# Performance work log

Measured on AMD Instinct MI355X. Metric: run time of the kernel, lower is better.

The kernel has to match this reference:

```python
import jax, jax.numpy as jnp
import numpy as np

NEG = -jnp.inf


def _pipeline(logits, presence_penalties, frequency_penalties, repetition_penalties,
              temperatures, top_p, min_p, top_a, tfs, typical_p,
              epsilon_cutoff, eta_cutoff, smoothing_factor, smoothing_curve,
              prompt_tokens, output_tokens, top_k):
    N, V = logits.shape
    rows = jnp.arange(N)[:, None]
    cols = jnp.arange(V)[None, :]

    # ---- presence / frequency / repetition penalties (bincount via scatter-add) ----
    pbin = jnp.zeros((N, V + 1), jnp.int32).at[rows, prompt_tokens].add(1)[:, :V]
    obin = jnp.zeros((N, V + 1), jnp.int32).at[rows, output_tokens].add(1)[:, :V]
    seen = (pbin > 0) | (obin > 0)
    rp = jnp.where(seen, repetition_penalties[:, None], 1.0)
    logits = jnp.where(logits > 0, logits / rp, logits * rp)
    logits = logits - frequency_penalties[:, None] * obin.astype(logits.dtype)
    logits = logits - presence_penalties[:, None] * (obin > 0).astype(logits.dtype)

    # ---- temperature ----
    logits = logits / temperatures[:, None]

    # ---- top-k + top-p (sort ascending, mask, unsort) ----
    order = jnp.argsort(logits, axis=-1)               # ascending
    ls = jnp.take_along_axis(logits, order, axis=-1)
    kth_pos = (V - jnp.clip(top_k.astype(jnp.int32), 1, V))[:, None]
    kth_val = jnp.take_along_axis(ls, kth_pos, axis=1)
    ls = jnp.where(ls < kth_val, NEG, ls)
    cs = jnp.cumsum(jax.nn.softmax(ls, axis=-1), axis=-1)
    pmask = (cs <= (1.0 - top_p)[:, None]).at[:, -1].set(False)
    ls = jnp.where(pmask, NEG, ls)
    logits = jnp.take_along_axis(ls, jnp.argsort(order, axis=-1), axis=-1)

    # ---- tail-free sampling (sort descending, 2nd-derivative CDF cutoff) ----
    order_d = jnp.argsort(-logits, axis=-1)            # descending order of logits
    ls = jnp.take_along_axis(logits, order_d, axis=-1)
    probs = jax.nn.softmax(ls, axis=-1)
    d2 = jnp.abs(jnp.diff(jnp.diff(probs, axis=-1), axis=-1))   # (N, V-2)
    cdf = jnp.cumsum(d2 / jnp.sum(d2, axis=-1, keepdims=True), axis=-1)
    m = cdf > tfs[:, None]
    m = jnp.concatenate([jnp.zeros((N, 1), bool), m, jnp.ones((N, 1), bool)], axis=-1)
    ls = jnp.where(m, NEG, ls)
    logits = jnp.take_along_axis(ls, jnp.argsort(order_d, axis=-1), axis=-1)

    # ---- eta cutoff (entropy-adaptive threshold, always keep argmax) ----
    sl = jax.nn.log_softmax(logits, axis=-1)
    probs = jnp.exp(sl)
    sl_safe = jnp.where(probs > 0, sl, 0.0)            # nansum equivalent
    neg_ent = jnp.sum(probs * sl_safe, axis=-1)
    eps = jnp.minimum(eta_cutoff, jnp.sqrt(eta_cutoff) * jnp.exp(neg_ent))[:, None]
    top_idx = jnp.argmax(probs, axis=-1)[:, None]
    logits = jnp.where((probs < eps) & (cols != top_idx), NEG, logits)

    # ---- epsilon cutoff (absolute prob threshold, always keep argmax) ----
    probs = jax.nn.softmax(logits, axis=-1)
    top_idx = jnp.argmax(probs, axis=-1)[:, None]
    logits = jnp.where((probs < epsilon_cutoff[:, None]) & (cols != top_idx), NEG, logits)

    # ---- locally typical sampling ----
    sl = jax.nn.log_softmax(logits, axis=-1)
    probs = jnp.exp(sl)
    sl_safe = jnp.where(probs > 0, sl, 0.0)
    neg_ent = jnp.sum(probs * sl_safe, axis=-1, keepdims=True)
    dev = jnp.abs(neg_ent - sl)                        # surprisal deviation
    order_t = jnp.argsort(dev, axis=-1)
    rp2 = jnp.take_along_axis(probs, order_t, axis=-1)
    msort = (jnp.cumsum(rp2, axis=-1) >= typical_p[:, None]).at[:, 0].set(False)
    mask = jnp.zeros((N, V), bool).at[rows, order_t].set(msort)
    logits = jnp.where(mask, NEG, logits)

    # ---- quadratic (smoothing) sampling ----
    mx = jnp.max(logits, axis=-1, keepdims=True)
    finite = logits != NEG
    diff = jnp.where(finite, logits, mx) - mx          # finite everywhere
    kq = (3.0 - smoothing_curve[:, None]) / 2.0
    sq = (smoothing_curve[:, None] - 1.0) / 2.0
    sfc = smoothing_factor[:, None]
    trans = -(kq * sfc * diff ** 2) + sq * sfc * diff ** 3 + mx
    trans = jnp.where(finite, trans, logits)
    logits = jnp.where(sfc > 0, trans, logits)

    # ---- min-p ----
    probs = jax.nn.softmax(logits, axis=-1)
    top_prob = jnp.max(probs, axis=-1, keepdims=True)
    logits = jnp.where(probs < min_p[:, None] * top_prob, NEG, logits)

    # ---- top-a ----
    probs = jax.nn.softmax(logits, axis=-1)
    top_prob = jnp.max(probs, axis=-1, keepdims=True)
    logits = jnp.where(probs < top_a[:, None] * top_prob ** 2, NEG, logits)

    return logits


def setup_inputs() -> dict:
    N, V, PL, OL = 256, 50257, 512, 128
    ks = jax.random.split(jax.random.key(0), 17)
    u = lambda k, lo, hi: lo + (hi - lo) * jax.random.uniform(k, (N,), jnp.float32)
    return {
        "logits": 3.0 * jax.random.normal(ks[0], (N, V), jnp.float32),
        "prompt_tokens": jax.random.randint(ks[1], (N, PL), 0, V),
        "output_tokens": jax.random.randint(ks[2], (N, OL), 0, V),
        "presence_penalties": u(ks[3], 0.0, 0.5),
        "frequency_penalties": u(ks[4], 0.0, 0.5),
        "repetition_penalties": u(ks[5], 1.0, 1.3),
        "temperatures": u(ks[6], 0.5, 1.5),
        "top_p": u(ks[7], 0.85, 0.99),
        "top_k": jax.random.randint(ks[8], (N,), 1, 2048, dtype=jnp.int32),
        "min_p": u(ks[9], 0.0, 0.05),
        "top_a": u(ks[10], 0.0, 0.1),
        "tfs": u(ks[11], 0.95, 0.999),
        "typical_p": u(ks[12], 0.9, 0.999),
        "epsilon_cutoff": u(ks[13], 1e-5, 1e-4),
        "eta_cutoff": u(ks[14], 1e-5, 1e-4),
        "smoothing_factor": u(ks[15], 0.05, 0.25),
        "smoothing_curve": u(ks[16], 1.0, 2.0),
    }


def reference(logits, prompt_tokens, output_tokens, presence_penalties,
              frequency_penalties, repetition_penalties, temperatures, top_p,
              top_k, min_p, top_a, tfs, typical_p, epsilon_cutoff, eta_cutoff,
              smoothing_factor, smoothing_curve):
    return _pipeline(logits, presence_penalties, frequency_penalties,
                     repetition_penalties, temperatures, top_p, min_p, top_a,
                     tfs, typical_p, epsilon_cutoff, eta_cutoff,
                     smoothing_factor, smoothing_curve,
                     prompt_tokens, output_tokens, top_k)
```

## Files before the change

### kernel.cpp

```cpp
#include <hip/hip_runtime.h>
#include <stdint.h>

#define TPB 1024
#define NWAVE 16
#define MAXK 2304
#define NV4 13
#define BIG_NEG (-1.0e30f)

__device__ __forceinline__ uint32_t fkey(float x) {
  uint32_t s = __float_as_uint(x);
  return (s & 0x80000000u) ? ~s : (s | 0x80000000u);
}
__device__ __forceinline__ float fkey_inv(uint32_t u) {
  uint32_t s = (u & 0x80000000u) ? (u & 0x7fffffffu) : ~u;
  return __uint_as_float(s);
}
__device__ __forceinline__ unsigned long long shfl_xor_u64(unsigned long long v, int m) {
  uint32_t lo = (uint32_t)v, hi = (uint32_t)(v >> 32);
  lo = (uint32_t)__shfl_xor((int)lo, m, 64);
  hi = (uint32_t)__shfl_xor((int)hi, m, 64);
  return (((unsigned long long)hi) << 32) | lo;
}

struct TokMem { uint32_t obin[12568]; uint32_t seen[1600]; };
struct SortMem { unsigned long long kp[4096]; };
union __align__(16) U1 { TokMem tok; SortMem srt; };

__device__ __forceinline__ float block_sum1(float v, float* buf) {
  int lane = threadIdx.x & 63, wd = threadIdx.x >> 6;
#pragma unroll
  for (int off = 32; off > 0; off >>= 1) v += __shfl_down(v, off, 64);
  if (lane == 0) buf[wd] = v;
  __syncthreads();
  const float4* b4 = (const float4*)buf;
  float4 A = b4[0], B = b4[1], C = b4[2], D = b4[3];
  float r = A.x; r += A.y; r += A.z; r += A.w;
  r += B.x; r += B.y; r += B.z; r += B.w;
  r += C.x; r += C.y; r += C.z; r += C.w;
  r += D.x; r += D.y; r += D.z; r += D.w;
  return r;
}

__device__ __forceinline__ float wbuf_prefix(const float* wbuf, int wd) {
  const float4* w4 = (const float4*)wbuf;
  float4 a = w4[0], b = w4[1], c = w4[2], d = w4[3];
  float t[16] = {a.x, a.y, a.z, a.w, b.x, b.y, b.z, b.w,
                 c.x, c.y, c.z, c.w, d.x, d.y, d.z, d.w};
  float base = 0.f;
#pragma unroll
  for (int i = 0; i < 16; ++i) base += (i < wd) ? t[i] : 0.f;
  return base;
}

__device__ __forceinline__ int wave_reduce_int(int v) {
#pragma unroll
  for (int off = 32; off > 0; off >>= 1) v += __shfl_down(v, off, 64);
  return __shfl(v, 0, 64);
}

template <class Pred>
__device__ __forceinline__ int wave_psearch(int lo, int hi, Pred pred) {
  const int lane = (int)threadIdx.x & 63;
  while (lo <= hi) {
    int range = hi - lo + 1;
    int stride = (range + 63) >> 6;
    long long p = (long long)lo + (long long)stride * lane;
    bool q = (p <= hi) ? pred((int)p) : false;
    unsigned long long bm = __ballot(q);
    int h = bm ? (63 - (int)__clzll(bm)) : -1;
    int nlo = (h >= 0) ? (int)((long long)lo + (long long)stride * h + 1) : lo;
    long long pf = (long long)lo + (long long)stride * (h + 1);
    int nhi = (pf <= (long long)hi) ? (int)pf - 1 : hi;
    if (nlo > nhi) return nlo;
    lo = nlo; hi = nhi;
  }
  return lo;
}

__device__ void block_scan3x3(const float* __restrict__ se, float* __restrict__ sp,
                              float* __restrict__ sq, float* __restrict__ sr, int m,
                              float* wA, float* wB, float* wC) {
  int tid = (int)threadIdx.x, lane = tid & 63, wd = tid >> 6;
  int b = tid * 3;
  __syncthreads();
  float e0 = (b     < m) ? se[b]     : 0.f;
  float e1 = (b + 1 < m) ? se[b + 1] : 0.f;
  float e2 = (b + 2 < m) ? se[b + 2] : 0.f;
  float e3 = (b + 3 < m) ? se[b + 3] : 0.f;
  float e4 = (b + 4 < m) ? se[b + 4] : 0.f;
  float q0 = (b     < m) ? sq[b]     : 0.f;
  float q1 = (b + 1 < m) ? sq[b + 1] : 0.f;
  float q2 = (b + 2 < m) ? sq[b + 2] : 0.f;
  float z0 = fabsf((e2 - e1) - (e1 - e0));
  float z1 = fabsf((e3 - e2) - (e2 - e1));
  float z2 = fabsf((e4 - e3) - (e3 - e2));
  float ae1 = e0 + e1, ae2 = ae1 + e2;
  float aq1 = q0 + q1, aq2 = aq1 + q2;
  float az1 = z0 + z1, az2 = az1 + z2;
  float tE = ae2, wE = ae2, tQ = aq2, wQ = aq2, tZ = az2, wZ = az2;
#pragma unroll
  for (int off = 1; off < 64; off <<= 1) {
    float sE = __shfl_up(wE, off, 64);
    float sQ = __shfl_up(wQ, off, 64);
    float sZ = __shfl_up(wZ, off, 64);
    if (lane >= off) { wE += sE; wQ += sQ; wZ += sZ; }
  }
  if (lane == 63) { wA[wd] = wE; wB[wd] = wQ; wC[wd] = wZ; }
  __syncthreads();
  float bE = wbuf_prefix(wA, wd), bQ = wbuf_prefix(wB, wd), bZ = wbuf_prefix(wC, wd);
  float xE = bE + (wE - tE), xQ = bQ + (wQ - tQ), xZ = bZ + (wZ - tZ);
  if (b < m)     { sp[b]     = e0 + xE;  sq[b]     = q0 + xQ;  sr[b]     = z0 + xZ; }
  if (b + 1 < m) { sp[b + 1] = ae1 + xE; sq[b + 1] = aq1 + xQ; sr[b + 1] = az1 + xZ; }
  if (b + 2 < m) { sp[b + 2] = ae2 + xE; sq[b + 2] = aq2 + xQ; sr[b + 2] = az2 + xZ; }
  __syncthreads();
}

__device__ uint32_t wave_select_digit2k(const uint32_t* __restrict__ h, uint32_t* w_io) {
  int lane = threadIdx.x & 63;
  uint32_t w = *w_io;
  const int base = lane << 5;
  uint32_t lsum = 0;
#pragma unroll
  for (int t = 0; t < 8; ++t) {
    const int tt = (t + lane) & 7;
    const uint4 v = *(const uint4*)(h + base + tt * 4);
    lsum += v.x + v.y + v.z + v.w;
  }
  uint32_t W = lsum;
#pragma unroll
  for (int off = 1; off < 64; off <<= 1) {
    uint32_t x = (uint32_t)__shfl_down((int)W, off, 64);
    if (lane + off < 64) W += x;
  }
  uint32_t Wn = (uint32_t)__shfl_down((int)W, 1, 64);
  if (lane == 63) Wn = 0;
  const bool isb = (W >= w) && (Wn < w);
  int dloc = -1; uint32_t wloc = 0;
  if (isb) {
    uint32_t sfx = Wn;
#pragma unroll
    for (int t = 31; t >= 0; --t) {
      uint32_t c = h[base + t];
      uint32_t si = sfx + c;
      if (si >= w && sfx < w) { dloc = base + t; wloc = w - sfx; }
      sfx = si;
    }
  }
  unsigned long long bm = __ballot(dloc >= 0);
  int src = (int)__popcll(bm - 1ull);
  uint32_t d = (uint32_t)__shfl(dloc, src, 64);
  *w_io = (uint32_t)__shfl((int)wloc, src, 64);
  return d;
}

__device__ uint32_t wave_select_digit256(const uint32_t* __restrict__ h, uint32_t* w_io) {
  int lane = threadIdx.x & 63;
  uint32_t w = *w_io;
  const uint4 v = ((const uint4*)h)[lane];
  uint32_t c0 = v.x, c1 = v.y, c2 = v.z, c3 = v.w;
  uint32_t t0 = c0 + c1 + c2 + c3;
  uint32_t W = t0;
#pragma unroll
  for (int off = 1; off < 64; off <<= 1) {
    uint32_t x = (uint32_t)__shfl_down((int)W, off, 64);
    if (lane + off < 64) W += x;
  }
  uint32_t Wn = (uint32_t)__shfl_down((int)W, 1, 64);
  if (lane == 63) Wn = 0;
  uint32_t S0 = W, S1 = W - c0, S2 = S1 - c1, S3 = S2 - c2, S4 = Wn;
  int dloc = -1; uint32_t wloc = 0;
  if (S0 >= w && S1 < w) { dloc = 4 * lane + 0; wloc = w - S1; }
  if (S1 >= w && S2 < w) { dloc = 4 * lane + 1; wloc = w - S2; }
  if (S2 >= w && S3 < w) { dloc = 4 * lane + 2; wloc = w - S3; }
  if (S3 >= w && S4 < w) { dloc = 4 * lane + 3; wloc = w - S4; }
  unsigned long long bm = __ballot(dloc >= 0);
  int src = (int)__popcll(bm - 1ull);
  uint32_t d = (uint32_t)__shfl(dloc, src, 64);
  *w_io = (uint32_t)__shfl((int)wloc, src, 64);
  return d;
}

template <int NE, bool PING>
__device__ void hybrid_sort(unsigned long long* kp, unsigned long long* kb1, int n) {
  const int tid = (int)threadIdx.x;
  unsigned long long k[NE];
#pragma unroll
  for (int e = 0; e < NE; ++e) {
    int i = e * TPB + tid;
    k[e] = (i < n) ? kp[i] : ~0ull;
  }
  int pb = 0;
  for (int kk = 2; kk <= n; kk <<= 1) {
    for (int j = kk >> 1; j > 0; j >>= 1) {
      if (j >= TPB) {
        const int em = j / TPB;
#pragma unroll
        for (int e = 0; e < NE; ++e) {
          if ((e & em) == 0 && (e + em) < NE) {
            int e2 = e + em;
            int i = e * TPB + tid;
            bool up = ((i & kk) == 0);
            if ((k[e] > k[e2]) == up) {
              unsigned long long tk = k[e]; k[e] = k[e2]; k[e2] = tk;
            }
          }
        }
      } else if (j >= 64) {
        unsigned long long* kb = (PING && pb) ? kb1 : kp;
#pragma unroll
        for (int e = 0; e < NE; ++e) {
          int i = e * TPB + tid;
          if (i < n) kb[i] = k[e];
        }
        __syncthreads();
#pragma unroll
        for (int e = 0; e < NE; ++e) {
          int i = e * TPB + tid;
          if (i < n) {
            unsigned long long o = kb[i ^ j];
            bool up = ((i & kk) == 0);
            bool lower = ((i & j) == 0);
            bool takeMin = (lower == up);
            bool takeOther = takeMin ? (o < k[e]) : (o > k[e]);
            if (takeOther) k[e] = o;
          }
        }
        if (PING) pb ^= 1;
        else __syncthreads();
      } else {
#pragma unroll
        for (int e = 0; e < NE; ++e) {
          int i = e * TPB + tid;
          unsigned long long o = shfl_xor_u64(k[e], j);
          bool up = ((i & kk) == 0);
          bool lower = ((i & j) == 0);
          bool takeMin = (lower == up);
          bool takeOther = takeMin ? (o < k[e]) : (o > k[e]);
          if (takeOther) k[e] = o;
        }
      }
    }
  }
  __syncthreads();
#pragma unroll
  for (int e = 0; e < NE; ++e) {
    int i = e * TPB + tid;
    if (i < n) kp[i] = k[e];
  }
  __syncthreads();
}

__device__ __forceinline__ uint32_t penal_val(float l, int j, bool sn,
    const uint32_t* __restrict__ obin,
    float f_rep, float inv_rep, float f_freq, float f_pres, float inv_temp) {
  int ob = 0;
  if (sn) ob = (int)((obin[j >> 2] >> (8 * (j & 3))) & 255u);
  l = (l > 0.0f) ? (l * (sn ? inv_rep : 1.0f)) : (l * (sn ? f_rep : 1.0f));
  l = l - f_freq * (float)ob;
  l = l - ((ob > 0) ? f_pres : 0.0f);
  l = l * inv_temp;
  return fkey(l);
}
__device__ __forceinline__ uint32_t penal_key(float l, int j,
    const uint32_t* __restrict__ seen, const uint32_t* __restrict__ obin,
    float f_rep, float inv_rep, float f_freq, float f_pres, float inv_temp) {
  bool sn = (seen[j >> 5] >> (j & 31)) & 1u;
  return penal_val(l, j, sn, obin, f_rep, inv_rep, f_freq, f_pres, inv_temp);
}

#define FOR_ELEMS(...) do {                                                   \
    if (tid < head) { int j = tid; uint32_t u = uh; (void)j; (void)u; __VA_ARGS__; } \
    _Pragma("unroll")                                                         \
    for (int s4_ = 0; s4_ < NV4; ++s4_) {                                     \
      int iv_ = s4_ * TPB + tid;                                              \
      if (iv_ < nvec) {                                                       \
        int jb_ = head + 4 * iv_;                                             \
        { int j = jb_ + 0; uint32_t u = uk[s4_ * 4 + 0]; (void)j; (void)u; __VA_ARGS__; } \
        { int j = jb_ + 1; uint32_t u = uk[s4_ * 4 + 1]; (void)j; (void)u; __VA_ARGS__; } \
        { int j = jb_ + 2; uint32_t u = uk[s4_ * 4 + 2]; (void)j; (void)u; __VA_ARGS__; } \
        { int j = jb_ + 3; uint32_t u = uk[s4_ * 4 + 3]; (void)j; (void)u; __VA_ARGS__; } \
      }                                                                       \
    }                                                                         \
    if (tid < ntail) { int j = head + 4 * nvec + tid; uint32_t u = ut; (void)j; (void)u; __VA_ARGS__; } \
  } while (0)

#define COLLECT_ELEM do {                                                     \
    bool pk_ = (u >= kth_u);                                                  \
    unsigned long long bm_ = __ballot(pk_);                                   \
    if (bm_) {                                                                \
      uint32_t base_ = 0;                                                     \
      if (lane == 0) base_ = atomicAdd(&s_cnt, (uint32_t)__popcll(bm_));      \
      base_ = (uint32_t)__shfl((int)base_, 0, 64);                            \
      if (pk_) {                                                              \
        uint32_t pos_ = base_ + (uint32_t)__popcll(bm_ & ((1ull << (unsigned)lane) - 1ull)); \
        if (pos_ < MAXK)                                                      \
          kp[pos_] = (((unsigned long long)(~u)) << 16) | (unsigned long long)(uint32_t)j; \
      }                                                                       \
    }                                                                         \
  } while (0)

__global__ __launch_bounds__(TPB, 4)
void sampler_kernel(const float* __restrict__ logits,
                    const int* __restrict__ ptoks, const int* __restrict__ otoks,
                    const float* __restrict__ pres, const float* __restrict__ freq,
                    const float* __restrict__ rep, const float* __restrict__ temp,
                    const float* __restrict__ topp, const int* __restrict__ topk,
                    const float* __restrict__ minp, const float* __restrict__ topa,
                    const float* __restrict__ tfsv, const float* __restrict__ typp,
                    const float* __restrict__ epsc, const float* __restrict__ etac,
                    const float* __restrict__ smf, const float* __restrict__ smc,
                    float* __restrict__ out, int N, int V, int PL, int OL) {
  __shared__ U1 u1;
  __shared__ __align__(16) uint32_t s_hist2k[2048];
  __shared__ __align__(16) uint32_t s_h256[256];
  __shared__ __align__(16) uint32_t s_h256b[256];
  __shared__ float s_e[MAXK];
  __shared__ float s_p[MAXK];
  __shared__ float s_q[MAXK];
  __shared__ float s_r[MAXK];
  __shared__ unsigned long long kb1[2048];
  __shared__ __align__(16) float s_site[12][NWAVE];
  __shared__ uint32_t s_cnt;
  __shared__ int s_K, s_ilo, s_ihi;

  const int tid = (int)threadIdx.x;
  const int r = (int)blockIdx.x;
  const int wd = tid >> 6;
  const int lane = tid & 63;

  const float* lrow = logits + (size_t)r * V;
  float* orow = out + (size_t)r * V;

  {
    const uint4 z4 = make_uint4(0u, 0u, 0u, 0u);
    uint4* ob4 = (uint4*)u1.tok.obin;
    for (int i = tid; i < 3142; i += TPB) ob4[i] = z4;
    uint4* se4 = (uint4*)u1.tok.seen;
    for (int i = tid; i < 400; i += TPB) se4[i] = z4;
    uint4* h4 = (uint4*)s_hist2k;
    for (int i = tid; i < 512; i += TPB) h4[i] = z4;
    if (tid < 64) ((uint4*)s_h256)[tid] = z4;
    else if (tid >= 64 && tid < 128) ((uint4*)s_h256b)[tid - 64] = z4;
  }
  if (tid == 0) s_cnt = 0;
  __syncthreads();
  for (int i = tid; i < PL; i += TPB) {
    int t = ptoks[(size_t)r * PL + i];
    if ((unsigned)t < (unsigned)V) atomicOr(&u1.tok.seen[t >> 5], 1u << (t & 31));
  }
  for (int i = tid; i < OL; i += TPB) {
    int t = otoks[(size_t)r * OL + i];
    if ((unsigned)t < (unsigned)V) {
      atomicOr(&u1.tok.seen[t >> 5], 1u << (t & 31));
      atomicAdd(&u1.tok.obin[t >> 2], 1u << (8 * (t & 3)));
    }
  }
  __syncthreads();

  const float f_pres = pres[r], f_freq = freq[r], f_rep = rep[r], f_temp = temp[r];
  const float f_topp = topp[r], f_minp = minp[r], f_topa = topa[r], f_tfs = tfsv[r];
  const float f_typp = typp[r], f_epsc = epsc[r], f_etac = etac[r];
  const float f_smf = smf[r], f_smc = smc[r];
  const float inv_rep = 1.0f / f_rep, inv_temp = 1.0f / f_temp;
  int k_topk = topk[r];
  if (k_topk < 1) k_topk = 1;
  if (k_topk > V) k_topk = V;

  const uint32_t* seenp = u1.tok.seen;
  const uint32_t* obinp = u1.tok.obin;

  uintptr_t ra = (uintptr_t)lrow;
  int head = (int)(((16u - (uint32_t)(ra & 15u)) & 15u) >> 2);
  if (head > V) head = V;
  const int nvec = (V - head) >> 2;
  const int ntail = V - head - (nvec << 2);

  uint32_t uk[NV4 * 4];
  uint32_t uh = 0, ut = 0;
#pragma unroll
  for (int s4 = 0; s4 < NV4; ++s4) {
    int iv = s4 * TPB + tid;
    uint32_t u0 = 0, u1k = 0, u2k = 0, u3 = 0;
    if (iv < nvec) {
      const float4 lv = *(const float4*)(lrow + head + 4 * iv);
      int jb = head + 4 * iv;
      uint32_t w0 = seenp[jb >> 5];
      uint32_t w1 = seenp[(jb >> 5) + 1];
      uint32_t sb = (uint32_t)(((((uint64_t)w1) << 32) | (uint64_t)w0) >> (jb & 31));
      u0 = penal_val(lv.x, jb + 0, (sb >> 0) & 1u, obinp, f_rep, inv_rep, f_freq, f_pres, inv_temp);
      u1k = penal_val(lv.y, jb + 1, (sb >> 1) & 1u, obinp, f_rep, inv_rep, f_freq, f_pres, inv_temp);
      u2k = penal_val(lv.z, jb + 2, (sb >> 2) & 1u, obinp, f_rep, inv_rep, f_freq, f_pres, inv_temp);
      u3 = penal_val(lv.w, jb + 3, (sb >> 3) & 1u, obinp, f_rep, inv_rep, f_freq, f_pres, inv_temp);
      atomicAdd(&s_hist2k[u0 >> 21], 1u);
      atomicAdd(&s_hist2k[u1k >> 21], 1u);
      atomicAdd(&s_hist2k[u2k >> 21], 1u);
      atomicAdd(&s_hist2k[u3 >> 21], 1u);
    }
    uk[s4 * 4 + 0] = u0; uk[s4 * 4 + 1] = u1k; uk[s4 * 4 + 2] = u2k; uk[s4 * 4 + 3] = u3;
  }
  if (tid < head) {
    uh = penal_key(lrow[tid], tid, seenp, obinp, f_rep, inv_rep, f_freq, f_pres, inv_temp);
    atomicAdd(&s_hist2k[uh >> 21], 1u);
  }
  if (tid < ntail) {
    int j = head + 4 * nvec + tid;
    ut = penal_key(lrow[j], j, seenp, obinp, f_rep, inv_rep, f_freq, f_pres, inv_temp);
    atomicAdd(&s_hist2k[ut >> 21], 1u);
  }

  {
    uintptr_t oa = (uintptr_t)orow;
    int ohead = (int)(((16u - (uint32_t)(oa & 15u)) & 15u) >> 2);
    if (ohead > V) ohead = V;
    int onvec = (V - ohead) >> 2;
    for (int j = tid; j < ohead; j += TPB) orow[j] = BIG_NEG;
    float4* o4 = (float4*)(orow + ohead);
    const float4 f4 = make_float4(BIG_NEG, BIG_NEG, BIG_NEG, BIG_NEG);
    for (int i = tid; i < onvec; i += TPB) o4[i] = f4;
    for (int j = ohead + (onvec << 2) + tid; j < V; j += TPB) orow[j] = BIG_NEG;
  }
  __syncthreads();

  uint32_t w = (uint32_t)k_topk;
  uint32_t d11 = wave_select_digit2k(s_hist2k, &w);
  FOR_ELEMS(if ((u >> 21) == d11) atomicAdd(&s_h256[(u >> 13) & 255u], 1u));
  __syncthreads();
  uint32_t d8 = wave_select_digit256(s_h256, &w);
  const uint32_t pref19 = (d11 << 8) | d8;
  FOR_ELEMS(if ((u >> 13) == pref19) atomicAdd(&s_h256b[(u >> 5) & 255u], 1u));
  __syncthreads();
  uint32_t d8c = wave_select_digit256(s_h256b, &w);
  const uint32_t kth_u = (d11 << 21) | (d8 << 13) | (d8c << 5);

  unsigned long long* kp = u1.srt.kp;
  FOR_ELEMS(COLLECT_ELEM);
  __syncthreads();
  int K = (int)s_cnt;
  if (K > MAXK) K = MAXK;

  {
    int n1 = 64; while (n1 < K) n1 <<= 1;
    for (int i = K + tid; i < n1; i += TPB) kp[i] = ~0ull;
    __syncthreads();
    if (n1 <= 1024) hybrid_sort<1, true>(kp, kb1, n1);
    else if (n1 == 2048) hybrid_sort<2, true>(kp, kb1, n1);
    else hybrid_sort<4, false>(kp, nullptr, n1);
  }

  if (wd == 0) {
    const uint32_t kth_inv = (uint32_t)(kp[k_topk - 1] >> 16);
    int KT = wave_psearch(0, K - 1, [&](int i) {
      return (uint32_t)(kp[i] >> 16) <= kth_inv;
    });
    if (lane == 0) s_K = KT;
  }
  __syncthreads();
  K = s_K;

  const float m0 = fkey_inv(~(uint32_t)(kp[0] >> 16));

  for (int i = tid; i < K; i += TPB) {
    float v = fkey_inv(~(uint32_t)(kp[i] >> 16));
    float e = __expf(v - m0);
    s_e[i] = e; s_q[i] = e * (v - m0);
  }
  block_scan3x3(s_e, s_p, s_q, s_r, K, s_site[7], s_site[8], s_site[9]);

  int i_lo = 0, i_hi = K - 1;
  if (wd == 0) {
    const float S = s_p[K - 1];

    const float thS = (1.0f - f_topp) * S;
    int cnt = 0;
    for (int i = lane; i < K; i += 64) {
      float ss = S - s_p[i] + s_e[i];
      if (i == 0 || ss > thS) cnt++;
    }
    int K1 = wave_reduce_int(cnt);

    auto dzAt = [&](int i, int mm) -> float {
      float x0 = s_e[i];
      float x1 = (i + 1 < mm) ? s_e[i + 1] : 0.f;
      float x2 = (i + 2 < mm) ? s_e[i + 2] : 0.f;
      return fabsf((x2 - x1) - (x1 - x0));
    };
    int K2;
    if (K1 >= 2) {
      float base = (K1 >= 3) ? s_r[K1 - 3] : 0.f;
      float rKm2 = base + dzAt(K1 - 2, K1);
      float rKm1 = rKm2 + dzAt(K1 - 1, K1);
      const float thT = f_tfs * rKm1;
      const int Km3 = K1 - 3;
      K2 = 1 + wave_psearch(0, K1 - 2, [&](int j) {
        float rj = (j <= Km3) ? s_r[j] : rKm2;
        return rj <= thT;
      });
    } else K2 = 1;

    const float SD = s_p[K2 - 1];
    const float neD = s_q[K2 - 1] / SD - __logf(SD);
    const float eps = fminf(f_etac, sqrtf(f_etac) * __expf(neD));
    const float thD = eps * SD;
    int K3 = wave_psearch(1, K2 - 1, [&](int i) { return s_e[i] >= thD; });

    const float thE = f_epsc * s_p[K3 - 1];
    int K4 = wave_psearch(1, K3 - 1, [&](int i) { return s_e[i] >= thE; });

    const float SF = s_p[K4 - 1];
    const float lseF = __logf(SF);
    const float neF = s_q[K4 - 1] / SF - lseF;
    const float vth = neF + lseF + m0;
    const float typSF = f_typp * SF;
    const int c = wave_psearch(0, K4 - 1, [&](int i) {
      return fkey_inv(~(uint32_t)(kp[i] >> 16)) >= vth;
    });
    const int nB = K4 - c;

    auto keyAt = [&](int i) -> unsigned long long {
      unsigned long long kk = kp[i];
      float v = fkey_inv(~(uint32_t)(kk >> 16));
      return (((unsigned long long)fkey(fabsf(v - vth))) << 16) | (kk & 0xffffull);
    };
    auto splitFor = [&](int p) -> int {
      int alo = p - nB; if (alo < 0) alo = 0;
      int ahi = (p < c) ? p : c;
      while (alo < ahi) {
        int am = (alo + ahi + 1) >> 1;
        int tb = p - am;
        bool take = true;
        if (tb < nB) take = (keyAt(c - am) <= keyAt(c + tb));
        if (take) alo = am; else ahi = am - 1;
      }
      return alo;
    };
    auto massLess = [&](int p) -> bool {
      int a = splitFor(p);
      int b = p - a;
      float sum = s_p[c + b - 1] - ((c - a > 0) ? s_p[c - a - 1] : 0.f);
      return sum < typSF;
    };
    int plo = 0, phi = K4;
    while (phi > plo) {
      int range = phi - plo;
      int stride = (range + 63) >> 6;
      int p = plo + stride * (lane + 1);
      bool q = false;
      if (p <= phi) q = massLess(p);
      unsigned long long bm = __ballot(q);
      int h = bm ? (63 - (int)__clzll(bm)) : -1;
      int nlo = (h >= 0) ? (plo + stride * (h + 1)) : plo;
      long long nf = (long long)plo + (long long)stride * (long long)(h + 2);
      int nhi = (nf <= (long long)phi) ? (int)nf - 1 : phi;
      plo = nlo; phi = nhi;
    }
    int L = plo;
    if (L < 1) L = 1;
    if (L > K4) L = K4;
    int a = splitFor(L);
    if (lane == 0) { s_ilo = c - a; s_ihi = c + (L - a) - 1; }
  }
  __syncthreads();
  i_lo = s_ilo; i_hi = s_ihi;

  float S2;
  const float mx = fkey_inv(~(uint32_t)(kp[i_lo] >> 16));
  {
    const float kq = (3.0f - f_smc) * 0.5f;
    const float sq = (f_smc - 1.0f) * 0.5f;
    float pS = 0.f;
    for (int i = i_lo + tid; i <= i_hi; i += TPB) {
      float v = fkey_inv(~(uint32_t)(kp[i] >> 16));
      float d = v - mx;
      float tr = mx - (kq * f_smf) * (d * d) + (sq * f_smf) * ((d * d) * d);
      float v2 = (f_smf > 0.0f) ? tr : v;
      float e = __expf(v2 - mx);
      s_q[i] = e;
      s_r[i] = v2;
      if (e >= f_minp) pS += e;
    }
    S2 = block_sum1(pS, s_site[6]);
  }

  {
    const float thA = f_topa / S2;
    for (int i = i_lo + tid; i <= i_hi; i += TPB) {
      float e = s_q[i];
      if (e >= f_minp && e >= thA) {
        int idx = (int)(kp[i] & 0xffffull);
        orow[idx] = s_r[i];
      }
    }
  }
}

extern "C" void kernel_launch(void* const* d_in, const int* in_sizes, int n_in,
                              void* d_out, int out_size, void* d_ws, size_t ws_size,
                              hipStream_t stream) {
  const float* logits = (const float*)d_in[0];
  const int* ptoks = (const int*)d_in[1];
  const int* otoks = (const int*)d_in[2];
  const float* pres = (const float*)d_in[3];
  const float* freq = (const float*)d_in[4];
  const float* rep  = (const float*)d_in[5];
  const float* temp = (const float*)d_in[6];
  const float* topp = (const float*)d_in[7];
  const int*   topk = (const int*)d_in[8];
  const float* minp = (const float*)d_in[9];
  const float* topa = (const float*)d_in[10];
  const float* tfsv = (const float*)d_in[11];
  const float* typp = (const float*)d_in[12];
  const float* epsc = (const float*)d_in[13];
  const float* etac = (const float*)d_in[14];
  const float* smf  = (const float*)d_in[15];
  const float* smc  = (const float*)d_in[16];

  int N = in_sizes[3];
  int V = in_sizes[0] / N;
  int PL = in_sizes[1] / N;
  int OL = in_sizes[2] / N;

  sampler_kernel<<<N, TPB, 0, stream>>>(logits, ptoks, otoks, pres, freq, rep, temp,
                                        topp, topk, minp, topa, tfsv, typp, epsc, etac,
                                        smf, smc, (float*)d_out, N, V, PL, OL);
}
```

Measured before the change: 72.67 us.

## Prefetch logits early, drop third radix pass, use per-thread prefix-sum collection

The row's logits and the first chunk of prompt/output tokens are now loaded into registers before the shared-memory zeroing and token-bin construction, so global load latency overlaps that setup. The third 8-bit radix refinement pass is removed, and the threshold uses only 19 bits. That saves one full pass over the elements plus a barrier, but may admit more candidates into the sort buffer. Candidate collection switches from per-element ballot plus atomic to a per-thread count, a wave prefix scan and a single atomic per wave. This adds a counting pass and extra register pressure from holding the float4 values.

```diff
diff --git a/kernel.cpp b/kernel.cpp
--- a/kernel.cpp
+++ b/kernel.cpp
@@ -261,12 +261,6 @@
   l = l * inv_temp;
   return fkey(l);
 }
-__device__ __forceinline__ uint32_t penal_key(float l, int j,
-    const uint32_t* __restrict__ seen, const uint32_t* __restrict__ obin,
-    float f_rep, float inv_rep, float f_freq, float f_pres, float inv_temp) {
-  bool sn = (seen[j >> 5] >> (j & 31)) & 1u;
-  return penal_val(l, j, sn, obin, f_rep, inv_rep, f_freq, f_pres, inv_temp);
-}
 
 #define FOR_ELEMS(...) do {                                                   \
     if (tid < head) { int j = tid; uint32_t u = uh; (void)j; (void)u; __VA_ARGS__; } \
@@ -284,21 +278,6 @@
     if (tid < ntail) { int j = head + 4 * nvec + tid; uint32_t u = ut; (void)j; (void)u; __VA_ARGS__; } \
   } while (0)
 
-#define COLLECT_ELEM do {                                                     \
-    bool pk_ = (u >= kth_u);                                                  \
-    unsigned long long bm_ = __ballot(pk_);                                   \
-    if (bm_) {                                                                \
-      uint32_t base_ = 0;                                                     \
-      if (lane == 0) base_ = atomicAdd(&s_cnt, (uint32_t)__popcll(bm_));      \
-      base_ = (uint32_t)__shfl((int)base_, 0, 64);                            \
-      if (pk_) {                                                              \
-        uint32_t pos_ = base_ + (uint32_t)__popcll(bm_ & ((1ull << (unsigned)lane) - 1ull)); \
-        if (pos_ < MAXK)                                                      \
-          kp[pos_] = (((unsigned long long)(~u)) << 16) | (unsigned long long)(uint32_t)j; \
-      }                                                                       \
-    }                                                                         \
-  } while (0)
-
 __global__ __launch_bounds__(TPB, 4)
 void sampler_kernel(const float* __restrict__ logits,
                     const int* __restrict__ ptoks, const int* __restrict__ otoks,
@@ -313,7 +292,6 @@
   __shared__ U1 u1;
   __shared__ __align__(16) uint32_t s_hist2k[2048];
   __shared__ __align__(16) uint32_t s_h256[256];
-  __shared__ __align__(16) uint32_t s_h256b[256];
   __shared__ float s_e[MAXK];
   __shared__ float s_p[MAXK];
   __shared__ float s_q[MAXK];
@@ -330,6 +308,34 @@
 
   const float* lrow = logits + (size_t)r * V;
   float* orow = out + (size_t)r * V;
+
+  uintptr_t ra = (uintptr_t)lrow;
+  int head = (int)(((16u - (uint32_t)(ra & 15u)) & 15u) >> 2);
+  if (head > V) head = V;
+  const int nvec = (V - head) >> 2;
+  const int ntail = V - head - (nvec << 2);
+
+  float4 lv[NV4];
+  float lh = 0.f, lt = 0.f;
+#pragma unroll
+  for (int s4 = 0; s4 < NV4; ++s4) {
+    int iv = s4 * TPB + tid;
+    if (iv < nvec) lv[s4] = *(const float4*)(lrow + head + 4 * iv);
+  }
+  if (tid < head) lh = lrow[tid];
+  if (tid < ntail) lt = lrow[head + 4 * nvec + tid];
+  int pt = -1, ot = -1;
+  if (tid < PL) pt = ptoks[(size_t)r * PL + tid];
+  if (tid < OL) ot = otoks[(size_t)r * OL + tid];
+
+  const float f_pres = pres[r], f_freq = freq[r], f_rep = rep[r], f_temp = temp[r];
+  const float f_topp = topp[r], f_minp = minp[r], f_topa = topa[r], f_tfs = tfsv[r];
+  const float f_typp = typp[r], f_epsc = epsc[r], f_etac = etac[r];
+  const float f_smf = smf[r], f_smc = smc[r];
+  const float inv_rep = 1.0f / f_rep, inv_temp = 1.0f / f_temp;
+  int k_topk = topk[r];
+  if (k_topk < 1) k_topk = 1;
+  if (k_topk > V) k_topk = V;
 
   {
     const uint4 z4 = make_uint4(0u, 0u, 0u, 0u);
@@ -340,15 +346,19 @@
     uint4* h4 = (uint4*)s_hist2k;
     for (int i = tid; i < 512; i += TPB) h4[i] = z4;
     if (tid < 64) ((uint4*)s_h256)[tid] = z4;
-    else if (tid >= 64 && tid < 128) ((uint4*)s_h256b)[tid - 64] = z4;
   }
   if (tid == 0) s_cnt = 0;
   __syncthreads();
-  for (int i = tid; i < PL; i += TPB) {
+  if ((unsigned)pt < (unsigned)V) atomicOr(&u1.tok.seen[pt >> 5], 1u << (pt & 31));
+  for (int i = TPB + tid; i < PL; i += TPB) {
     int t = ptoks[(size_t)r * PL + i];
     if ((unsigned)t < (unsigned)V) atomicOr(&u1.tok.seen[t >> 5], 1u << (t & 31));
   }
-  for (int i = tid; i < OL; i += TPB) {
+  if ((unsigned)ot < (unsigned)V) {
+    atomicOr(&u1.tok.seen[ot >> 5], 1u << (ot & 31));
+    atomicAdd(&u1.tok.obin[ot >> 2], 1u << (8 * (ot & 3)));
+  }
+  for (int i = TPB + tid; i < OL; i += TPB) {
     int t = otoks[(size_t)r * OL + i];
     if ((unsigned)t < (unsigned)V) {
       atomicOr(&u1.tok.seen[t >> 5], 1u << (t & 31));
@@ -357,23 +367,8 @@
   }
   __syncthreads();
 
-  const float f_pres = pres[r], f_freq = freq[r], f_rep = rep[r], f_temp = temp[r];
-  const float f_topp = topp[r], f_minp = minp[r], f_topa = topa[r], f_tfs = tfsv[r];
-  const float f_typp = typp[r], f_epsc = epsc[r], f_etac = etac[r];
-  const float f_smf = smf[r], f_smc = smc[r];
-  const float inv_rep = 1.0f / f_rep, inv_temp = 1.0f / f_temp;
-  int k_topk = topk[r];
-  if (k_topk < 1) k_topk = 1;
-  if (k_topk > V) k_topk = V;
-
   const uint32_t* seenp = u1.tok.seen;
   const uint32_t* obinp = u1.tok.obin;
-
-  uintptr_t ra = (uintptr_t)lrow;
-  int head = (int)(((16u - (uint32_t)(ra & 15u)) & 15u) >> 2);
-  if (head > V) head = V;
-  const int nvec = (V - head) >> 2;
-  const int ntail = V - head - (nvec << 2);
 
   uint32_t uk[NV4 * 4];
   uint32_t uh = 0, ut = 0;
@@ -382,15 +377,15 @@
     int iv = s4 * TPB + tid;
     uint32_t u0 = 0, u1k = 0, u2k = 0, u3 = 0;
     if (iv < nvec) {
-      const float4 lv = *(const float4*)(lrow + head + 4 * iv);
+      const float4 lvv = lv[s4];
       int jb = head + 4 * iv;
       uint32_t w0 = seenp[jb >> 5];
       uint32_t w1 = seenp[(jb >> 5) + 1];
       uint32_t sb = (uint32_t)(((((uint64_t)w1) << 32) | (uint64_t)w0) >> (jb & 31));
-      u0 = penal_val(lv.x, jb + 0, (sb >> 0) & 1u, obinp, f_rep, inv_rep, f_freq, f_pres, inv_temp);
-      u1k = penal_val(lv.y, jb + 1, (sb >> 1) & 1u, obinp, f_rep, inv_rep, f_freq, f_pres, inv_temp);
-      u2k = penal_val(lv.z, jb + 2, (sb >> 2) & 1u, obinp, f_rep, inv_rep, f_freq, f_pres, inv_temp);
-      u3 = penal_val(lv.w, jb + 3, (sb >> 3) & 1u, obinp, f_rep, inv_rep, f_freq, f_pres, inv_temp);
+      u0 = penal_val(lvv.x, jb + 0, (sb >> 0) & 1u, obinp, f_rep, inv_rep, f_freq, f_pres, inv_temp);
+      u1k = penal_val(lvv.y, jb + 1, (sb >> 1) & 1u, obinp, f_rep, inv_rep, f_freq, f_pres, inv_temp);
+      u2k = penal_val(lvv.z, jb + 2, (sb >> 2) & 1u, obinp, f_rep, inv_rep, f_freq, f_pres, inv_temp);
+      u3 = penal_val(lvv.w, jb + 3, (sb >> 3) & 1u, obinp, f_rep, inv_rep, f_freq, f_pres, inv_temp);
       atomicAdd(&s_hist2k[u0 >> 21], 1u);
       atomicAdd(&s_hist2k[u1k >> 21], 1u);
       atomicAdd(&s_hist2k[u2k >> 21], 1u);
@@ -398,14 +393,17 @@
     }
     uk[s4 * 4 + 0] = u0; uk[s4 * 4 + 1] = u1k; uk[s4 * 4 + 2] = u2k; uk[s4 * 4 + 3] = u3;
   }
-  if (tid < head) {
-    uh = penal_key(lrow[tid], tid, seenp, obinp, f_rep, inv_rep, f_freq, f_pres, inv_temp);
-    atomicAdd(&s_hist2k[uh >> 21], 1u);
-  }
-  if (tid < ntail) {
-    int j = head + 4 * nvec + tid;
-    ut = penal_key(lrow[j], j, seenp, obinp, f_rep, inv_rep, f_freq, f_pres, inv_temp);
-    atomicAdd(&s_hist2k[ut >> 21], 1u);
+  {
+    bool snh = false, snt = false;
+    if (tid < head) snh = (seenp[tid >> 5] >> (tid & 31)) & 1u;
+    if (tid < head)
+      uh = penal_val(lh, tid, snh, obinp, f_rep, inv_rep, f_freq, f_pres, inv_temp);
+    if (tid < head) atomicAdd(&s_hist2k[uh >> 21], 1u);
+    int jt = head + 4 * nvec + tid;
+    if (tid < ntail) snt = (seenp[jt >> 5] >> (jt & 31)) & 1u;
+    if (tid < ntail)
+      ut = penal_val(lt, jt, snt, obinp, f_rep, inv_rep, f_freq, f_pres, inv_temp);
+    if (tid < ntail) atomicAdd(&s_hist2k[ut >> 21], 1u);
   }
 
   {
@@ -426,14 +424,30 @@
   FOR_ELEMS(if ((u >> 21) == d11) atomicAdd(&s_h256[(u >> 13) & 255u], 1u));
   __syncthreads();
   uint32_t d8 = wave_select_digit256(s_h256, &w);
-  const uint32_t pref19 = (d11 << 8) | d8;
-  FOR_ELEMS(if ((u >> 13) == pref19) atomicAdd(&s_h256b[(u >> 5) & 255u], 1u));
-  __syncthreads();
-  uint32_t d8c = wave_select_digit256(s_h256b, &w);
-  const uint32_t kth_u = (d11 << 21) | (d8 << 13) | (d8c << 5);
+  const uint32_t kth_u = (d11 << 21) | (d8 << 13);
 
   unsigned long long* kp = u1.srt.kp;
-  FOR_ELEMS(COLLECT_ELEM);
+  {
+    int cnt_t = 0;
+    FOR_ELEMS(cnt_t += (u >= kth_u) ? 1 : 0);
+    int incl = cnt_t;
+#pragma unroll
+    for (int off = 1; off < 64; off <<= 1) {
+      int x = __shfl_up(incl, off, 64);
+      if (lane >= off) incl += x;
+    }
+    int wtot = __shfl(incl, 63, 64);
+    uint32_t base = 0;
+    if (lane == 0 && wtot > 0) base = atomicAdd(&s_cnt, (uint32_t)wtot);
+    base = (uint32_t)__shfl((int)base, 0, 64);
+    uint32_t off_t = base + (uint32_t)(incl - cnt_t);
+    FOR_ELEMS(
+      if (u >= kth_u) {
+        if (off_t < MAXK)
+          kp[off_t] = (((unsigned long long)(~u)) << 16) | (unsigned long long)(uint32_t)j;
+        off_t++;
+      });
+  }
   __syncthreads();
   int K = (int)s_cnt;
   if (K > MAXK) K = MAXK;
```

Result: faster. 70.75 us (-2.6%).
